# Performance work log

Measured on AMD Instinct MI355X. Metric: run time of the kernel, lower is better.

Reference implementation:

```python
import jax, jax.numpy as jnp
import numpy as np
import math

CHANNELS = 128
NUM_NODES = 170
LENGTH = 12
BATCH = 128


def setup_inputs() -> dict:
    key = jax.random.key(0)
    k_x, k_es = jax.random.split(key)
    x = jax.random.normal(k_x, (BATCH, CHANNELS, NUM_NODES, LENGTH), dtype=jnp.float32)
    # xavier_uniform for E_s [channels, num_nodes]
    bound = math.sqrt(6.0 / (CHANNELS + NUM_NODES))
    E_s = jax.random.uniform(k_es, (CHANNELS, NUM_NODES), dtype=jnp.float32,
                             minval=-bound, maxval=bound)
    return {"x": x, "E_s": E_s}


def reference(x, E_s):
    # x: [B, C, N, T], E_s: [C, M] with M == N (num_nodes)
    # Note: the original also computes E_t = x * E_tod**2, which is dead code
    # (never used in the returned value), so it is omitted here.
    C = x.shape[1]
    # node embeddings: sum over channel and time -> [B, N, M]
    E_d = jnp.tanh(jnp.einsum('bcnt,cm->bnm', x, E_s))
    # node-node similarity: contract over the M (embedding) axis -> [B, N, N]
    scores = jax.nn.relu(jnp.einsum('bnm,bkm->bnk', E_d, E_d) / jnp.sqrt(jnp.float32(C)))
    A_adp = jax.nn.softmax(scores, axis=-1)  # [B, N, N]
    A_mean = A_adp.mean(axis=0)              # [N, N]
    return (A_mean > 0.5).astype(jnp.float32)
```

## Files before the change

### kernel.cpp

```cpp
#include <hip/hip_runtime.h>
#include <math.h>

#define NB 128
#define NC 128
#define NN 170
#define NT 12
#define MP 176
#define BSROW 196

#define ESP_SZ (NC * MP)
#define ED_SZ  (NB * NN * MP)
#define P_SZ   (NB * NN * MP)
#define PM_SZ  (8 * NN * NN)

typedef _Float16 h8 __attribute__((ext_vector_type(8)));
typedef _Float16 h4 __attribute__((ext_vector_type(4)));
typedef __fp16   g2 __attribute__((ext_vector_type(2)));
typedef float    f4 __attribute__((ext_vector_type(4)));

__device__ __forceinline__ float fast_tanh(float x) {
    float cx = fminf(fmaxf(x, -15.f), 15.f);
    float e  = __expf(2.f * cx);
    return (e - 1.f) * __builtin_amdgcn_rcpf(e + 1.f);
}

__global__ __launch_bounds__(256) void k0_pad_es(const float* __restrict__ Es,
                                                 float* __restrict__ Esp) {
    int idx = blockIdx.x * 256 + threadIdx.x;
    if (idx < ESP_SZ) {
        int c = idx / MP, m = idx % MP;
        Esp[idx] = (m < NN) ? Es[c * NN + m] : 0.f;
    }
}

__global__ __launch_bounds__(256) void k2_fused(const float* __restrict__ x,
                                                const float* __restrict__ Esp,
                                                float* __restrict__ Ed) {
    const int b = blockIdx.y, n0 = blockIdx.x * 32;
    const int t = threadIdx.x, tx = t & 15, ty = t >> 4;
    __shared__ __align__(16) float As[16][36];
    __shared__ __align__(16) float Bs[16][BSROW];

    float acc[2][12] = {};
    for (int c0 = 0; c0 < NC; c0 += 16) {
        __syncthreads();
        {
            int c  = t >> 4;
            int nn = (t & 15) * 2;
            #pragma unroll
            for (int u = 0; u < 2; ++u) {
                int n = n0 + nn + u;
                float s = 0.f;
                if (n < NN) {
                    const float4* p = reinterpret_cast<const float4*>(
                        x + ((size_t)((b * NC + c0 + c) * NN) + n) * NT);
                    float4 f0 = p[0], f1 = p[1], f2 = p[2];
                    s = ((f0.x + f0.y) + (f0.z + f0.w))
                      + ((f1.x + f1.y) + (f1.z + f1.w))
                      + ((f2.x + f2.y) + (f2.z + f2.w));
                }
                As[c][nn + u] = s;
            }
        }
        #pragma unroll
        for (int it = 0; it < 3; ++it) {
            int idx = t + it * 256;
            int c = idx / 48, mq = idx - c * 48;
            float4 v = make_float4(0.f, 0.f, 0.f, 0.f);
            if (mq < 44)
                v = *reinterpret_cast<const float4*>(Esp + (c0 + c) * MP + mq * 4);
            *reinterpret_cast<float4*>(&Bs[c][mq * 4]) = v;
        }
        __syncthreads();
        #pragma unroll
        for (int cc = 0; cc < 16; ++cc) {
            float2 av = *reinterpret_cast<const float2*>(&As[cc][ty * 2]);
            float a[2] = {av.x, av.y};
            float bb[12];
            #pragma unroll
            for (int off = 0; off < 3; ++off) {
                float4 bv = *reinterpret_cast<const float4*>(&Bs[cc][tx * 4 + off * 64]);
                bb[off * 4 + 0] = bv.x; bb[off * 4 + 1] = bv.y;
                bb[off * 4 + 2] = bv.z; bb[off * 4 + 3] = bv.w;
            }
            #pragma unroll
            for (int ii = 0; ii < 2; ++ii)
                #pragma unroll
                for (int jj = 0; jj < 12; ++jj)
                    acc[ii][jj] = fmaf(a[ii], bb[jj], acc[ii][jj]);
        }
    }
    #pragma unroll
    for (int ii = 0; ii < 2; ++ii) {
        int n = n0 + ty * 2 + ii;
        if (n >= NN) continue;
        float* Erow = Ed + ((size_t)(b * NN + n)) * MP;
        #pragma unroll
        for (int off = 0; off < 3; ++off) {
            int m = tx * 4 + off * 64;
            if (m >= MP) continue;
            float4 v;
            v.x = fast_tanh(acc[ii][off * 4 + 0]);
            v.y = fast_tanh(acc[ii][off * 4 + 1]);
            v.z = fast_tanh(acc[ii][off * 4 + 2]);
            v.w = fast_tanh(acc[ii][off * 4 + 3]);
            *reinterpret_cast<float4*>(Erow + m) = v;
        }
    }
}

__global__ __launch_bounds__(256) void k3_scores_mfma(const float* __restrict__ Ed,
                                                      float* __restrict__ P) {
    const int b = blockIdx.y, r0 = blockIdx.x * 32;
    const int t = threadIdx.x;
    const int lane = t & 63, wave = t >> 6;
    const int l15 = lane & 15, quad = lane >> 4;

    __shared__ __align__(16) _Float16 Eh[192 * 40];
    __shared__ __align__(16) float    Sc[32 * 204];

    const float* __restrict__ Edb = Ed + (size_t)b * NN * MP;

    f4 acc[2][3] = {};
    for (int mc = 0; mc < 192; mc += 32) {
        __syncthreads();
        #pragma unroll
        for (int it = 0; it < 6; ++it) {
            int idx = t + it * 256;
            int row = idx >> 3, q = idx & 7;
            float4 v = make_float4(0.f, 0.f, 0.f, 0.f);
            int col = mc + q * 4;
            if (row < NN && col < MP)
                v = *reinterpret_cast<const float4*>(Edb + (size_t)row * MP + col);
            g2 lo = __builtin_amdgcn_cvt_pkrtz(v.x, v.y);
            g2 hi = __builtin_amdgcn_cvt_pkrtz(v.z, v.w);
            h4 h;
            h[0] = (_Float16)lo[0]; h[1] = (_Float16)lo[1];
            h[2] = (_Float16)hi[0]; h[3] = (_Float16)hi[1];
            *reinterpret_cast<h4*>(&Eh[row * 40 + q * 4]) = h;
        }
        __syncthreads();
        const int ko = quad * 8;
        h8 a0 = *reinterpret_cast<const h8*>(&Eh[(r0 + l15) * 40 + ko]);
        h8 a1 = *reinterpret_cast<const h8*>(&Eh[(r0 + 16 + l15) * 40 + ko]);
        #pragma unroll
        for (int ci = 0; ci < 3; ++ci) {
            int kc = (wave * 3 + ci) * 16 + l15;
            h8 bf = *reinterpret_cast<const h8*>(&Eh[kc * 40 + ko]);
            acc[0][ci] = __builtin_amdgcn_mfma_f32_16x16x32_f16(a0, bf, acc[0][ci], 0, 0, 0);
            acc[1][ci] = __builtin_amdgcn_mfma_f32_16x16x32_f16(a1, bf, acc[1][ci], 0, 0, 0);
        }
    }

    const float scale = 0.08838834764831845f;
    #pragma unroll
    for (int rt = 0; rt < 2; ++rt)
        #pragma unroll
        for (int ci = 0; ci < 3; ++ci) {
            int col = (wave * 3 + ci) * 16 + l15;
            #pragma unroll
            for (int reg = 0; reg < 4; ++reg) {
                int rloc = rt * 16 + quad * 4 + reg;
                Sc[rloc * 204 + col] = fmaxf(acc[rt][ci][reg] * scale, 0.f);
            }
        }
    __syncthreads();

    for (int rr = 0; rr < 8; ++rr) {
        int r = wave * 8 + rr;
        int n = r0 + r;
        if (n >= NN) continue;
        float v0 = Sc[r * 204 + lane];
        float v1 = Sc[r * 204 + lane + 64];
        int  k2i = lane + 128;
        bool has2 = (k2i < NN);
        float v2 = has2 ? Sc[r * 204 + k2i] : -1.f;
        float m = fmaxf(fmaxf(v0, v1), v2);
        #pragma unroll
        for (int off = 32; off; off >>= 1) m = fmaxf(m, __shfl_xor(m, off, 64));
        float e0 = __expf(v0 - m);
        float e1 = __expf(v1 - m);
        float e2 = has2 ? __expf(v2 - m) : 0.f;
        float s = e0 + e1 + e2;
        #pragma unroll
        for (int off = 32; off; off >>= 1) s += __shfl_xor(s, off, 64);
        float inv = 1.f / s;
        float* Pr = P + ((size_t)(b * NN + n)) * MP;
        Pr[lane]      = e0 * inv;
        Pr[lane + 64] = e1 * inv;
        if (has2) Pr[k2i] = e2 * inv;
    }
}

__global__ __launch_bounds__(256) void k4a_partial(const float* __restrict__ P,
                                                   float* __restrict__ Pm) {
    int p = blockIdx.x * 256 + threadIdx.x;
    if (p >= NN * NN) return;
    int n = p / NN, k = p - n * NN;
    const float* base = P + (size_t)blockIdx.y * 16 * NN * MP + (size_t)n * MP + k;
    float s = 0.f;
    #pragma unroll
    for (int b = 0; b < 16; ++b) s += base[(size_t)b * NN * MP];
    Pm[blockIdx.y * (NN * NN) + p] = s;
}

__global__ __launch_bounds__(256) void k4b_thresh(const float* __restrict__ Pm,
                                                  float* __restrict__ out) {
    int p = blockIdx.x * 256 + threadIdx.x;
    if (p >= NN * NN) return;
    float s = 0.f;
    #pragma unroll
    for (int g = 0; g < 8; ++g) s += Pm[g * (NN * NN) + p];
    out[p] = (s * (1.f / 128.f) > 0.5f) ? 1.f : 0.f;
}

extern "C" void kernel_launch(void* const* d_in, const int* in_sizes, int n_in,
                              void* d_out, int out_size, void* d_ws, size_t ws_size,
                              hipStream_t stream) {
    const float* x  = (const float*)d_in[0];
    const float* Es = (const float*)d_in[1];
    float* out = (float*)d_out;
    float* wsf = (float*)d_ws;

    float* Esp = wsf;
    float* Ed  = wsf + ESP_SZ;
    float* P   = wsf + ESP_SZ + ED_SZ;
    float* Pm  = wsf + ESP_SZ + ED_SZ + P_SZ;

    k0_pad_es<<<88, 256, 0, stream>>>(Es, Esp);
    k2_fused<<<dim3(6, 128), 256, 0, stream>>>(x, Esp, Ed);
    k3_scores_mfma<<<dim3(6, 128), 256, 0, stream>>>(Ed, P);
    k4a_partial<<<dim3(113, 8), 256, 0, stream>>>(P, Pm);
    k4b_thresh<<<113, 256, 0, stream>>>(Pm, out);
}
```

Measured before the change: 235.4 us.

## Store intermediates in fp16, drop Es padding kernel, merge mean-threshold reductions

```diff
diff --git a/kernel.cpp b/kernel.cpp
--- a/kernel.cpp
+++ b/kernel.cpp
@@ -8,10 +8,8 @@
 #define MP 176
 #define BSROW 196
 
-#define ESP_SZ (NC * MP)
-#define ED_SZ  (NB * NN * MP)
-#define P_SZ   (NB * NN * MP)
-#define PM_SZ  (8 * NN * NN)
+#define ED_SZ ((size_t)NB * NN * MP)
+#define P_SZ  ((size_t)NB * NN * MP)
 
 typedef _Float16 h8 __attribute__((ext_vector_type(8)));
 typedef _Float16 h4 __attribute__((ext_vector_type(4)));
@@ -24,18 +22,9 @@
     return (e - 1.f) * __builtin_amdgcn_rcpf(e + 1.f);
 }
 
-__global__ __launch_bounds__(256) void k0_pad_es(const float* __restrict__ Es,
-                                                 float* __restrict__ Esp) {
-    int idx = blockIdx.x * 256 + threadIdx.x;
-    if (idx < ESP_SZ) {
-        int c = idx / MP, m = idx % MP;
-        Esp[idx] = (m < NN) ? Es[c * NN + m] : 0.f;
-    }
-}
-
 __global__ __launch_bounds__(256) void k2_fused(const float* __restrict__ x,
-                                                const float* __restrict__ Esp,
-                                                float* __restrict__ Ed) {
+                                                const float* __restrict__ Es,
+                                                _Float16* __restrict__ Ed) {
     const int b = blockIdx.y, n0 = blockIdx.x * 32;
     const int t = threadIdx.x, tx = t & 15, ty = t >> 4;
     __shared__ __align__(16) float As[16][36];
@@ -63,13 +52,10 @@
             }
         }
         #pragma unroll
-        for (int it = 0; it < 3; ++it) {
+        for (int it = 0; it < 11; ++it) {
             int idx = t + it * 256;
-            int c = idx / 48, mq = idx - c * 48;
-            float4 v = make_float4(0.f, 0.f, 0.f, 0.f);
-            if (mq < 44)
-                v = *reinterpret_cast<const float4*>(Esp + (c0 + c) * MP + mq * 4);
-            *reinterpret_cast<float4*>(&Bs[c][mq * 4]) = v;
+            int c = idx / 176, m = idx - c * 176;
+            Bs[c][m] = (m < NN) ? Es[(c0 + c) * NN + m] : 0.f;
         }
         __syncthreads();
         #pragma unroll
@@ -94,23 +80,25 @@
     for (int ii = 0; ii < 2; ++ii) {
         int n = n0 + ty * 2 + ii;
         if (n >= NN) continue;
-        float* Erow = Ed + ((size_t)(b * NN + n)) * MP;
+        _Float16* Erow = Ed + ((size_t)(b * NN + n)) * MP;
         #pragma unroll
         for (int off = 0; off < 3; ++off) {
             int m = tx * 4 + off * 64;
             if (m >= MP) continue;
-            float4 v;
-            v.x = fast_tanh(acc[ii][off * 4 + 0]);
-            v.y = fast_tanh(acc[ii][off * 4 + 1]);
-            v.z = fast_tanh(acc[ii][off * 4 + 2]);
-            v.w = fast_tanh(acc[ii][off * 4 + 3]);
-            *reinterpret_cast<float4*>(Erow + m) = v;
-        }
-    }
-}
-
-__global__ __launch_bounds__(256) void k3_scores_mfma(const float* __restrict__ Ed,
-                                                      float* __restrict__ P) {
+            g2 lo = __builtin_amdgcn_cvt_pkrtz(fast_tanh(acc[ii][off * 4 + 0]),
+                                               fast_tanh(acc[ii][off * 4 + 1]));
+            g2 hi = __builtin_amdgcn_cvt_pkrtz(fast_tanh(acc[ii][off * 4 + 2]),
+                                               fast_tanh(acc[ii][off * 4 + 3]));
+            h4 hv;
+            hv[0] = (_Float16)lo[0]; hv[1] = (_Float16)lo[1];
+            hv[2] = (_Float16)hi[0]; hv[3] = (_Float16)hi[1];
+            *reinterpret_cast<h4*>(Erow + m) = hv;
+        }
+    }
+}
+
+__global__ __launch_bounds__(256) void k3_scores_mfma(const _Float16* __restrict__ Ed,
+                                                      _Float16* __restrict__ P) {
     const int b = blockIdx.y, r0 = blockIdx.x * 32;
     const int t = threadIdx.x;
     const int lane = t & 63, wave = t >> 6;
@@ -119,25 +107,20 @@
     __shared__ __align__(16) _Float16 Eh[192 * 40];
     __shared__ __align__(16) float    Sc[32 * 204];
 
-    const float* __restrict__ Edb = Ed + (size_t)b * NN * MP;
+    const _Float16* __restrict__ Edb = Ed + (size_t)b * NN * MP;
 
     f4 acc[2][3] = {};
     for (int mc = 0; mc < 192; mc += 32) {
         __syncthreads();
         #pragma unroll
-        for (int it = 0; it < 6; ++it) {
+        for (int it = 0; it < 3; ++it) {
             int idx = t + it * 256;
-            int row = idx >> 3, q = idx & 7;
-            float4 v = make_float4(0.f, 0.f, 0.f, 0.f);
-            int col = mc + q * 4;
+            int row = idx >> 2, q = idx & 3;
+            int col = mc + q * 8;
+            h8 v = {};
             if (row < NN && col < MP)
-                v = *reinterpret_cast<const float4*>(Edb + (size_t)row * MP + col);
-            g2 lo = __builtin_amdgcn_cvt_pkrtz(v.x, v.y);
-            g2 hi = __builtin_amdgcn_cvt_pkrtz(v.z, v.w);
-            h4 h;
-            h[0] = (_Float16)lo[0]; h[1] = (_Float16)lo[1];
-            h[2] = (_Float16)hi[0]; h[3] = (_Float16)hi[1];
-            *reinterpret_cast<h4*>(&Eh[row * 40 + q * 4]) = h;
+                v = *reinterpret_cast<const h8*>(Edb + (size_t)row * MP + col);
+            *reinterpret_cast<h8*>(&Eh[row * 40 + q * 8]) = v;
         }
         __syncthreads();
         const int ko = quad * 8;
@@ -185,32 +168,28 @@
         #pragma unroll
         for (int off = 32; off; off >>= 1) s += __shfl_xor(s, off, 64);
         float inv = 1.f / s;
-        float* Pr = P + ((size_t)(b * NN + n)) * MP;
-        Pr[lane]      = e0 * inv;
-        Pr[lane + 64] = e1 * inv;
-        if (has2) Pr[k2i] = e2 * inv;
-    }
-}
-
-__global__ __launch_bounds__(256) void k4a_partial(const float* __restrict__ P,
-                                                   float* __restrict__ Pm) {
+        _Float16* Pr = P + ((size_t)(b * NN + n)) * MP;
+        Pr[lane]      = (_Float16)(e0 * inv);
+        Pr[lane + 64] = (_Float16)(e1 * inv);
+        if (has2) Pr[k2i] = (_Float16)(e2 * inv);
+    }
+}
+
+__global__ __launch_bounds__(256) void k4_mean_thresh(const _Float16* __restrict__ P,
+                                                      float* __restrict__ out) {
     int p = blockIdx.x * 256 + threadIdx.x;
     if (p >= NN * NN) return;
     int n = p / NN, k = p - n * NN;
-    const float* base = P + (size_t)blockIdx.y * 16 * NN * MP + (size_t)n * MP + k;
-    float s = 0.f;
+    const _Float16* base = P + (size_t)n * MP + k;
+    float s0 = 0.f, s1 = 0.f, s2 = 0.f, s3 = 0.f;
     #pragma unroll
-    for (int b = 0; b < 16; ++b) s += base[(size_t)b * NN * MP];
-    Pm[blockIdx.y * (NN * NN) + p] = s;
-}
-
-__global__ __launch_bounds__(256) void k4b_thresh(const float* __restrict__ Pm,
-                                                  float* __restrict__ out) {
-    int p = blockIdx.x * 256 + threadIdx.x;
-    if (p >= NN * NN) return;
-    float s = 0.f;
-    #pragma unroll
-    for (int g = 0; g < 8; ++g) s += Pm[g * (NN * NN) + p];
+    for (int b = 0; b < NB; b += 4) {
+        s0 += (float)base[(size_t)(b + 0) * NN * MP];
+        s1 += (float)base[(size_t)(b + 1) * NN * MP];
+        s2 += (float)base[(size_t)(b + 2) * NN * MP];
+        s3 += (float)base[(size_t)(b + 3) * NN * MP];
+    }
+    float s = (s0 + s1) + (s2 + s3);
     out[p] = (s * (1.f / 128.f) > 0.5f) ? 1.f : 0.f;
 }
 
@@ -220,16 +199,11 @@
     const float* x  = (const float*)d_in[0];
     const float* Es = (const float*)d_in[1];
     float* out = (float*)d_out;
-    float* wsf = (float*)d_ws;
-
-    float* Esp = wsf;
-    float* Ed  = wsf + ESP_SZ;
-    float* P   = wsf + ESP_SZ + ED_SZ;
-    float* Pm  = wsf + ESP_SZ + ED_SZ + P_SZ;
-
-    k0_pad_es<<<88, 256, 0, stream>>>(Es, Esp);
-    k2_fused<<<dim3(6, 128), 256, 0, stream>>>(x, Esp, Ed);
+
+    _Float16* Ed = (_Float16*)d_ws;
+    _Float16* P  = Ed + ED_SZ;
+
+    k2_fused<<<dim3(6, 128), 256, 0, stream>>>(x, Es, Ed);
     k3_scores_mfma<<<dim3(6, 128), 256, 0, stream>>>(Ed, P);
-    k4a_partial<<<dim3(113, 8), 256, 0, stream>>>(P, Pm);
-    k4b_thresh<<<113, 256, 0, stream>>>(Pm, out);
-}
+    k4_mean_thresh<<<113, 256, 0, stream>>>(P, out);
+}
```

Result: slower. 253.9 us (+7.9%).
